# Kernel optimization log

Measured on AMD Instinct MI355X. Metric: run time of the kernel, lower is better.

The kernel has to match this reference:

```python
import jax, jax.numpy as jnp
import numpy as np
from jax import lax

SEQ, BATCH, IN, HID = 2048, 256, 64, 128


def setup_inputs() -> dict:
    key = jax.random.key(0)
    ks = jax.random.split(key, 5)
    return {
        "x": jax.random.normal(ks[0], (SEQ, BATCH, IN), dtype=jnp.float32),
        "Wx": jax.random.normal(ks[1], (HID, IN), dtype=jnp.float32) * 0.1,
        "bx": jax.random.normal(ks[2], (HID,), dtype=jnp.float32) * 0.1,
        "Wh": jax.random.normal(ks[3], (HID, HID), dtype=jnp.float32) * 0.1,
        "bh": jax.random.normal(ks[4], (HID,), dtype=jnp.float32) * 0.1,
    }


def reference(x, Wx, bx, Wh, bh):
    # Precompute the input projection for all timesteps in one GEMM:
    # fc_x(x[t]) + bh folded in. Shape (S, B, H).
    xp = jnp.einsum("sbi,hi->sbh", x, Wx) + bx + bh

    def step(h, xt):
        # h: (B, H); fc_h(h) = h @ Wh^T (bias folded into xp)
        h_new = jnp.tanh(h @ Wh.T + xt)
        return h_new, h_new

    h0 = jnp.zeros((x.shape[1], Wh.shape[0]), dtype=x.dtype)
    _, h_seq = lax.scan(step, h0, xp)  # (S, B, H)
    return h_seq, h_seq[-1][None]  # ((S,B,H), (1,B,H))
```

## Files before the change

### kernel.cpp

```cpp
#include <hip/hip_runtime.h>

#define SEQ   2048
#define BATCH 256
#define INDIM 64
#define HID   128

struct F2 { float x, y; };

template <int CTRL>
__device__ __forceinline__ float dpp_get(float v) {
    int t = __builtin_amdgcn_update_dpp(0, __builtin_bit_cast(int, v),
                                        CTRL, 0xF, 0xF, true);
    return __builtin_bit_cast(float, t);
}

#define PK_MUL(d, a, b) asm("v_pk_mul_f32 %0, %1, %2"     : "=v"(d) : "v"(a), "v"(b))
#define PK_FMA(d, a, b) asm("v_pk_fma_f32 %0, %1, %2, %0" : "+v"(d) : "v"(a), "v"(b))

#define TANH_K (-2.885390081777927f)
__device__ __forceinline__ float tanh_pre(float d, float bias_k) {
    float m = __builtin_fmaf(d, TANH_K, bias_k);
    float e = __builtin_amdgcn_exp2f(m);
    return (1.0f - e) * __builtin_amdgcn_rcpf(1.0f + e);
}

__global__ __launch_bounds__(512)
__attribute__((amdgpu_waves_per_eu(2, 2)))
void rnn_fused(
    const float* __restrict__ x,
    const float* __restrict__ Wx,
    const float* __restrict__ bx,
    const float* __restrict__ Wh,
    const float* __restrict__ bh,
    float* __restrict__ out)
{
    const int b   = blockIdx.x;
    const int tid = threadIdx.x;
    const int l   = tid & 63;
    const int w   = tid >> 6;
    const int s   = l & 15;
    const int j0  = w * 16 + (l >> 4) * 4;

    __shared__ __align__(16) float hbuf[2][HID];

    const double* WhD = (const double*)Wh;
    const double* WxD = (const double*)Wx;
    double wA[4], wB[4], wC[4], wD[4], wX[4], wY[4];
#pragma unroll
    for (int o = 0; o < 4; ++o) {
        const int row = j0 + (o ^ (l & 3));
        const int r   = row * 64 + 2 * s;
        wA[o] = WhD[r];      wB[o] = WhD[r + 1];
        wC[o] = WhD[r + 32]; wD[o] = WhD[r + 33];
        const int rx  = row * 32 + 2 * s;
        wX[o] = WxD[rx];     wY[o] = WxD[rx + 1];
    }
    const int jj = j0 + (l & 3);
    float bias_k = (bx[jj] + bh[jj]) * TANH_K;

    if (tid < 256) hbuf[tid >> 7][tid & 127] = 0.0f;
    __syncthreads();

    const double2* xb2 = (const double2*)(x + (size_t)b * INDIM + 4 * s);
    const size_t   S2  = (size_t)BATCH * INDIM / 4;
    double2 xa[4], xn[4];
#pragma unroll
    for (int i = 0; i < 4; ++i) xa[i] = xb2[(size_t)i * S2];

    float* outp = out + (size_t)b * HID + jj;
    const bool wr = (s < 4);
    float hv = 0.0f;

    for (int tb = 0; tb < SEQ; tb += 4) {
        asm volatile("" : "+v"(wA[0]), "+v"(wA[1]), "+v"(wA[2]), "+v"(wA[3]));
        asm volatile("" : "+v"(wB[0]), "+v"(wB[1]), "+v"(wB[2]), "+v"(wB[3]));
        asm volatile("" : "+v"(wC[0]), "+v"(wC[1]), "+v"(wC[2]), "+v"(wC[3]));
        asm volatile("" : "+v"(wD[0]), "+v"(wD[1]), "+v"(wD[2]), "+v"(wD[3]));
        asm volatile("" : "+v"(wX[0]), "+v"(wX[1]), "+v"(wX[2]), "+v"(wX[3]));
        asm volatile("" : "+v"(wY[0]), "+v"(wY[1]), "+v"(wY[2]), "+v"(wY[3]));
        asm volatile("" : "+v"(bias_k));

#pragma unroll
        for (int i = 0; i < 4; ++i) {
            int tp = tb + 4 + i; if (tp > SEQ - 1) tp = SEQ - 1;
            xn[i] = xb2[(size_t)tp * S2];
        }

#pragma unroll
        for (int q = 0; q < 4; ++q) {
            const double2* hbd = (const double2*)&hbuf[q & 1][0];

            const double2 H0 = hbd[s];
            const double2 H1 = hbd[16 + s];
            const double2 X  = xa[q];

            double acc0, acc1, acc2, acc3;
            PK_MUL(acc0, X.x, wX[0]); PK_MUL(acc1, X.x, wX[1]);
            PK_MUL(acc2, X.x, wX[2]); PK_MUL(acc3, X.x, wX[3]);
            PK_FMA(acc0, X.y, wY[0]); PK_FMA(acc1, X.y, wY[1]);
            PK_FMA(acc2, X.y, wY[2]); PK_FMA(acc3, X.y, wY[3]);
            PK_FMA(acc0, H0.x, wA[0]); PK_FMA(acc1, H0.x, wA[1]);
            PK_FMA(acc2, H0.x, wA[2]); PK_FMA(acc3, H0.x, wA[3]);
            PK_FMA(acc0, H0.y, wB[0]); PK_FMA(acc1, H0.y, wB[1]);
            PK_FMA(acc2, H0.y, wB[2]); PK_FMA(acc3, H0.y, wB[3]);
            PK_FMA(acc0, H1.x, wC[0]); PK_FMA(acc1, H1.x, wC[1]);
            PK_FMA(acc2, H1.x, wC[2]); PK_FMA(acc3, H1.x, wC[3]);
            PK_FMA(acc0, H1.y, wD[0]); PK_FMA(acc1, H1.y, wD[1]);
            PK_FMA(acc2, H1.y, wD[2]); PK_FMA(acc3, H1.y, wD[3]);

            float a0, a1, a2, a3;
            { F2 u = __builtin_bit_cast(F2, acc0); a0 = u.x + u.y; }
            { F2 u = __builtin_bit_cast(F2, acc1); a1 = u.x + u.y; }
            { F2 u = __builtin_bit_cast(F2, acc2); a2 = u.x + u.y; }
            { F2 u = __builtin_bit_cast(F2, acc3); a3 = u.x + u.y; }

            float c0 = a0 + dpp_get<0xB1>(a1);
            float c1 = a2 + dpp_get<0xB1>(a3);
            float d  = c0 + dpp_get<0x4E>(c1);
            d += dpp_get<0x124>(d);
            d += dpp_get<0x128>(d);

            hv = tanh_pre(d, bias_k);

            if (wr) {
                hbuf[(q + 1) & 1][jj] = hv;
                *outp = hv;
            }
            outp += BATCH * HID;

            asm volatile("s_waitcnt lgkmcnt(0)" ::: "memory");
            asm volatile("s_barrier" ::: "memory");
        }

#pragma unroll
        for (int i = 0; i < 4; ++i) xa[i] = xn[i];
    }

    if (wr)
        out[(size_t)SEQ * BATCH * HID + (size_t)b * HID + jj] = hv;
}

extern "C" void kernel_launch(void* const* d_in, const int* in_sizes, int n_in,
                              void* d_out, int out_size, void* d_ws, size_t ws_size,
                              hipStream_t stream) {
    const float* x  = (const float*)d_in[0];
    const float* Wx = (const float*)d_in[1];
    const float* bx = (const float*)d_in[2];
    const float* Wh = (const float*)d_in[3];
    const float* bh = (const float*)d_in[4];
    float* out = (float*)d_out;
    (void)in_sizes; (void)n_in; (void)d_ws; (void)ws_size; (void)out_size;
    rnn_fused<<<dim3(BATCH), dim3(512), 0, stream>>>(x, Wx, bx, Wh, bh, out);
}
```

Baseline: 607.8 us.

## Process two batch rows per block to share register-resident weights

Each block now handles two batch elements, interleaving their independent FMA chains, reductions and tanh so the same register-held Wh/Wx weights serve both rows, and launches half as many blocks. This aims to raise instruction-level parallelism inside the latency-bound serial recurrence and to cut the per-step barrier cost per batch row. The trade-off is twice the per-step arithmetic per block and higher register pressure, with only 128 blocks on a device that has 256 CUs, so part of the GPU sits idle.

```diff
diff --git a/kernel.cpp b/kernel.cpp
--- a/kernel.cpp
+++ b/kernel.cpp
@@ -34,14 +34,14 @@
     const float* __restrict__ bh,
     float* __restrict__ out)
 {
-    const int b   = blockIdx.x;
+    const int b0  = blockIdx.x * 2;
     const int tid = threadIdx.x;
     const int l   = tid & 63;
     const int w   = tid >> 6;
     const int s   = l & 15;
     const int j0  = w * 16 + (l >> 4) * 4;
 
-    __shared__ __align__(16) float hbuf[2][HID];
+    __shared__ __align__(16) float hbuf[2][2][HID];
 
     const double* WhD = (const double*)Wh;
     const double* WxD = (const double*)Wx;
@@ -58,18 +58,22 @@
     const int jj = j0 + (l & 3);
     float bias_k = (bx[jj] + bh[jj]) * TANH_K;
 
-    if (tid < 256) hbuf[tid >> 7][tid & 127] = 0.0f;
+    ((float*)hbuf)[tid] = 0.0f;
     __syncthreads();
 
-    const double2* xb2 = (const double2*)(x + (size_t)b * INDIM + 4 * s);
-    const size_t   S2  = (size_t)BATCH * INDIM / 4;
-    double2 xa[4], xn[4];
+    const double2* xb2a = (const double2*)(x + (size_t)b0 * INDIM + 4 * s);
+    const double2* xb2b = (const double2*)(x + (size_t)(b0 + 1) * INDIM + 4 * s);
+    const size_t   S2   = (size_t)BATCH * INDIM / 4;
+    double2 xaA[4], xnA[4], xaB[4], xnB[4];
 #pragma unroll
-    for (int i = 0; i < 4; ++i) xa[i] = xb2[(size_t)i * S2];
+    for (int i = 0; i < 4; ++i) {
+        xaA[i] = xb2a[(size_t)i * S2];
+        xaB[i] = xb2b[(size_t)i * S2];
+    }
 
-    float* outp = out + (size_t)b * HID + jj;
+    float* outp = out + (size_t)b0 * HID + jj;
     const bool wr = (s < 4);
-    float hv = 0.0f;
+    float hvA = 0.0f, hvB = 0.0f;
 
     for (int tb = 0; tb < SEQ; tb += 4) {
         asm volatile("" : "+v"(wA[0]), "+v"(wA[1]), "+v"(wA[2]), "+v"(wA[3]));
@@ -83,48 +87,78 @@
 #pragma unroll
         for (int i = 0; i < 4; ++i) {
             int tp = tb + 4 + i; if (tp > SEQ - 1) tp = SEQ - 1;
-            xn[i] = xb2[(size_t)tp * S2];
+            xnA[i] = xb2a[(size_t)tp * S2];
+            xnB[i] = xb2b[(size_t)tp * S2];
         }
 
 #pragma unroll
         for (int q = 0; q < 4; ++q) {
-            const double2* hbd = (const double2*)&hbuf[q & 1][0];
+            const double2* hbdA = (const double2*)&hbuf[0][q & 1][0];
+            const double2* hbdB = (const double2*)&hbuf[1][q & 1][0];
 
-            const double2 H0 = hbd[s];
-            const double2 H1 = hbd[16 + s];
-            const double2 X  = xa[q];
+            const double2 H0A = hbdA[s];
+            const double2 H1A = hbdA[16 + s];
+            const double2 H0B = hbdB[s];
+            const double2 H1B = hbdB[16 + s];
+            const double2 XA  = xaA[q];
+            const double2 XB  = xaB[q];
 
-            double acc0, acc1, acc2, acc3;
-            PK_MUL(acc0, X.x, wX[0]); PK_MUL(acc1, X.x, wX[1]);
-            PK_MUL(acc2, X.x, wX[2]); PK_MUL(acc3, X.x, wX[3]);
-            PK_FMA(acc0, X.y, wY[0]); PK_FMA(acc1, X.y, wY[1]);
-            PK_FMA(acc2, X.y, wY[2]); PK_FMA(acc3, X.y, wY[3]);
-            PK_FMA(acc0, H0.x, wA[0]); PK_FMA(acc1, H0.x, wA[1]);
-            PK_FMA(acc2, H0.x, wA[2]); PK_FMA(acc3, H0.x, wA[3]);
-            PK_FMA(acc0, H0.y, wB[0]); PK_FMA(acc1, H0.y, wB[1]);
-            PK_FMA(acc2, H0.y, wB[2]); PK_FMA(acc3, H0.y, wB[3]);
-            PK_FMA(acc0, H1.x, wC[0]); PK_FMA(acc1, H1.x, wC[1]);
-            PK_FMA(acc2, H1.x, wC[2]); PK_FMA(acc3, H1.x, wC[3]);
-            PK_FMA(acc0, H1.y, wD[0]); PK_FMA(acc1, H1.y, wD[1]);
-            PK_FMA(acc2, H1.y, wD[2]); PK_FMA(acc3, H1.y, wD[3]);
+            double pa0, pa1, pa2, pa3;
+            double pb0, pb1, pb2, pb3;
+            PK_MUL(pa0, XA.x, wX[0]); PK_MUL(pb0, XB.x, wX[0]);
+            PK_MUL(pa1, XA.x, wX[1]); PK_MUL(pb1, XB.x, wX[1]);
+            PK_MUL(pa2, XA.x, wX[2]); PK_MUL(pb2, XB.x, wX[2]);
+            PK_MUL(pa3, XA.x, wX[3]); PK_MUL(pb3, XB.x, wX[3]);
+            PK_FMA(pa0, XA.y, wY[0]); PK_FMA(pb0, XB.y, wY[0]);
+            PK_FMA(pa1, XA.y, wY[1]); PK_FMA(pb1, XB.y, wY[1]);
+            PK_FMA(pa2, XA.y, wY[2]); PK_FMA(pb2, XB.y, wY[2]);
+            PK_FMA(pa3, XA.y, wY[3]); PK_FMA(pb3, XB.y, wY[3]);
+            PK_FMA(pa0, H0A.x, wA[0]); PK_FMA(pb0, H0B.x, wA[0]);
+            PK_FMA(pa1, H0A.x, wA[1]); PK_FMA(pb1, H0B.x, wA[1]);
+            PK_FMA(pa2, H0A.x, wA[2]); PK_FMA(pb2, H0B.x, wA[2]);
+            PK_FMA(pa3, H0A.x, wA[3]); PK_FMA(pb3, H0B.x, wA[3]);
+            PK_FMA(pa0, H0A.y, wB[0]); PK_FMA(pb0, H0B.y, wB[0]);
+            PK_FMA(pa1, H0A.y, wB[1]); PK_FMA(pb1, H0B.y, wB[1]);
+            PK_FMA(pa2, H0A.y, wB[2]); PK_FMA(pb2, H0B.y, wB[2]);
+            PK_FMA(pa3, H0A.y, wB[3]); PK_FMA(pb3, H0B.y, wB[3]);
+            PK_FMA(pa0, H1A.x, wC[0]); PK_FMA(pb0, H1B.x, wC[0]);
+            PK_FMA(pa1, H1A.x, wC[1]); PK_FMA(pb1, H1B.x, wC[1]);
+            PK_FMA(pa2, H1A.x, wC[2]); PK_FMA(pb2, H1B.x, wC[2]);
+            PK_FMA(pa3, H1A.x, wC[3]); PK_FMA(pb3, H1B.x, wC[3]);
+            PK_FMA(pa0, H1A.y, wD[0]); PK_FMA(pb0, H1B.y, wD[0]);
+            PK_FMA(pa1, H1A.y, wD[1]); PK_FMA(pb1, H1B.y, wD[1]);
+            PK_FMA(pa2, H1A.y, wD[2]); PK_FMA(pb2, H1B.y, wD[2]);
+            PK_FMA(pa3, H1A.y, wD[3]); PK_FMA(pb3, H1B.y, wD[3]);
 
-            float a0, a1, a2, a3;
-            { F2 u = __builtin_bit_cast(F2, acc0); a0 = u.x + u.y; }
-            { F2 u = __builtin_bit_cast(F2, acc1); a1 = u.x + u.y; }
-            { F2 u = __builtin_bit_cast(F2, acc2); a2 = u.x + u.y; }
-            { F2 u = __builtin_bit_cast(F2, acc3); a3 = u.x + u.y; }
+            float aA0, aA1, aA2, aA3, aB0, aB1, aB2, aB3;
+            { F2 u = __builtin_bit_cast(F2, pa0); aA0 = u.x + u.y; }
+            { F2 u = __builtin_bit_cast(F2, pa1); aA1 = u.x + u.y; }
+            { F2 u = __builtin_bit_cast(F2, pa2); aA2 = u.x + u.y; }
+            { F2 u = __builtin_bit_cast(F2, pa3); aA3 = u.x + u.y; }
+            { F2 u = __builtin_bit_cast(F2, pb0); aB0 = u.x + u.y; }
+            { F2 u = __builtin_bit_cast(F2, pb1); aB1 = u.x + u.y; }
+            { F2 u = __builtin_bit_cast(F2, pb2); aB2 = u.x + u.y; }
+            { F2 u = __builtin_bit_cast(F2, pb3); aB3 = u.x + u.y; }
 
-            float c0 = a0 + dpp_get<0xB1>(a1);
-            float c1 = a2 + dpp_get<0xB1>(a3);
-            float d  = c0 + dpp_get<0x4E>(c1);
-            d += dpp_get<0x124>(d);
-            d += dpp_get<0x128>(d);
+            float cA0 = aA0 + dpp_get<0xB1>(aA1);
+            float cB0 = aB0 + dpp_get<0xB1>(aB1);
+            float cA1 = aA2 + dpp_get<0xB1>(aA3);
+            float cB1 = aB2 + dpp_get<0xB1>(aB3);
+            float dA  = cA0 + dpp_get<0x4E>(cA1);
+            float dB  = cB0 + dpp_get<0x4E>(cB1);
+            dA += dpp_get<0x124>(dA);
+            dB += dpp_get<0x124>(dB);
+            dA += dpp_get<0x128>(dA);
+            dB += dpp_get<0x128>(dB);
 
-            hv = tanh_pre(d, bias_k);
+            hvA = tanh_pre(dA, bias_k);
+            hvB = tanh_pre(dB, bias_k);
 
             if (wr) {
-                hbuf[(q + 1) & 1][jj] = hv;
-                *outp = hv;
+                hbuf[0][(q + 1) & 1][jj] = hvA;
+                hbuf[1][(q + 1) & 1][jj] = hvB;
+                *outp        = hvA;
+                *(outp + HID) = hvB;
             }
             outp += BATCH * HID;
 
@@ -133,11 +167,13 @@
         }
 
 #pragma unroll
-        for (int i = 0; i < 4; ++i) xa[i] = xn[i];
+        for (int i = 0; i < 4; ++i) { xaA[i] = xnA[i]; xaB[i] = xnB[i]; }
     }
 
-    if (wr)
-        out[(size_t)SEQ * BATCH * HID + (size_t)b * HID + jj] = hv;
+    if (wr) {
+        out[(size_t)SEQ * BATCH * HID + (size_t)b0 * HID + jj]       = hvA;
+        out[(size_t)SEQ * BATCH * HID + (size_t)(b0 + 1) * HID + jj] = hvB;
+    }
 }
 
 extern "C" void kernel_launch(void* const* d_in, const int* in_sizes, int n_in,
@@ -150,5 +186,5 @@
     const float* bh = (const float*)d_in[4];
     float* out = (float*)d_out;
     (void)in_sizes; (void)n_in; (void)d_ws; (void)ws_size; (void)out_size;
-    rnn_fused<<<dim3(BATCH), dim3(512), 0, stream>>>(x, Wx, bx, Wh, bh, out);
+    rnn_fused<<<dim3(BATCH / 2), dim3(512), 0, stream>>>(x, Wx, bx, Wh, bh, out);
 }
```

New measurement: 1.095 ms. 80.2% more time.

## Halve block size so each thread computes two hidden outputs per step

Applied to the files above, without the earlier changes.

The work split changes from 512 threads with 4 output rows per 16-lane group to 256 threads with 8 rows, so each lane computes two hidden units per timestep. With 4 waves per block instead of 8, the per-step s_barrier has fewer waves to synchronize. The cost is double the register footprint for weights (96 VGPR doubles) and twice the serial FMA work per lane on the latency-critical recurrent path. Occupancy is now pinned at 1 wave per EU.

```diff
diff --git a/kernel.cpp b/kernel.cpp
--- a/kernel.cpp
+++ b/kernel.cpp
@@ -24,8 +24,8 @@
     return (1.0f - e) * __builtin_amdgcn_rcpf(1.0f + e);
 }
 
-__global__ __launch_bounds__(512)
-__attribute__((amdgpu_waves_per_eu(2, 2)))
+__global__ __launch_bounds__(256)
+__attribute__((amdgpu_waves_per_eu(1, 1)))
 void rnn_fused(
     const float* __restrict__ x,
     const float* __restrict__ Wx,
@@ -39,26 +39,27 @@
     const int l   = tid & 63;
     const int w   = tid >> 6;
     const int s   = l & 15;
-    const int j0  = w * 16 + (l >> 4) * 4;
+    const int j0  = w * 32 + (l >> 4) * 8;
 
     __shared__ __align__(16) float hbuf[2][HID];
 
     const double* WhD = (const double*)Wh;
     const double* WxD = (const double*)Wx;
-    double wA[4], wB[4], wC[4], wD[4], wX[4], wY[4];
+    double wA[8], wB[8], wC[8], wD[8], wX[8], wY[8];
 #pragma unroll
-    for (int o = 0; o < 4; ++o) {
-        const int row = j0 + (o ^ (l & 3));
+    for (int o = 0; o < 8; ++o) {
+        const int row = j0 + (o & 4) + ((o & 3) ^ (l & 3));
         const int r   = row * 64 + 2 * s;
         wA[o] = WhD[r];      wB[o] = WhD[r + 1];
         wC[o] = WhD[r + 32]; wD[o] = WhD[r + 33];
         const int rx  = row * 32 + 2 * s;
         wX[o] = WxD[rx];     wY[o] = WxD[rx + 1];
     }
-    const int jj = j0 + (l & 3);
-    float bias_k = (bx[jj] + bh[jj]) * TANH_K;
+    const int jj  = j0 + (l & 3);
+    float bias_k  = (bx[jj]     + bh[jj])     * TANH_K;
+    float bias_k2 = (bx[jj + 4] + bh[jj + 4]) * TANH_K;
 
-    if (tid < 256) hbuf[tid >> 7][tid & 127] = 0.0f;
+    ((float*)hbuf)[tid] = 0.0f;
     __syncthreads();
 
     const double2* xb2 = (const double2*)(x + (size_t)b * INDIM + 4 * s);
@@ -69,16 +70,22 @@
 
     float* outp = out + (size_t)b * HID + jj;
     const bool wr = (s < 4);
-    float hv = 0.0f;
+    float hv1 = 0.0f, hv2 = 0.0f;
 
     for (int tb = 0; tb < SEQ; tb += 4) {
-        asm volatile("" : "+v"(wA[0]), "+v"(wA[1]), "+v"(wA[2]), "+v"(wA[3]));
-        asm volatile("" : "+v"(wB[0]), "+v"(wB[1]), "+v"(wB[2]), "+v"(wB[3]));
-        asm volatile("" : "+v"(wC[0]), "+v"(wC[1]), "+v"(wC[2]), "+v"(wC[3]));
-        asm volatile("" : "+v"(wD[0]), "+v"(wD[1]), "+v"(wD[2]), "+v"(wD[3]));
-        asm volatile("" : "+v"(wX[0]), "+v"(wX[1]), "+v"(wX[2]), "+v"(wX[3]));
-        asm volatile("" : "+v"(wY[0]), "+v"(wY[1]), "+v"(wY[2]), "+v"(wY[3]));
-        asm volatile("" : "+v"(bias_k));
+        asm volatile("" : "+v"(wA[0]), "+v"(wA[1]), "+v"(wA[2]), "+v"(wA[3]),
+                          "+v"(wA[4]), "+v"(wA[5]), "+v"(wA[6]), "+v"(wA[7]));
+        asm volatile("" : "+v"(wB[0]), "+v"(wB[1]), "+v"(wB[2]), "+v"(wB[3]),
+                          "+v"(wB[4]), "+v"(wB[5]), "+v"(wB[6]), "+v"(wB[7]));
+        asm volatile("" : "+v"(wC[0]), "+v"(wC[1]), "+v"(wC[2]), "+v"(wC[3]),
+                          "+v"(wC[4]), "+v"(wC[5]), "+v"(wC[6]), "+v"(wC[7]));
+        asm volatile("" : "+v"(wD[0]), "+v"(wD[1]), "+v"(wD[2]), "+v"(wD[3]),
+                          "+v"(wD[4]), "+v"(wD[5]), "+v"(wD[6]), "+v"(wD[7]));
+        asm volatile("" : "+v"(wX[0]), "+v"(wX[1]), "+v"(wX[2]), "+v"(wX[3]),
+                          "+v"(wX[4]), "+v"(wX[5]), "+v"(wX[6]), "+v"(wX[7]));
+        asm volatile("" : "+v"(wY[0]), "+v"(wY[1]), "+v"(wY[2]), "+v"(wY[3]),
+                          "+v"(wY[4]), "+v"(wY[5]), "+v"(wY[6]), "+v"(wY[7]));
+        asm volatile("" : "+v"(bias_k), "+v"(bias_k2));
 
 #pragma unroll
         for (int i = 0; i < 4; ++i) {
@@ -94,37 +101,49 @@
             const double2 H1 = hbd[16 + s];
             const double2 X  = xa[q];
 
-            double acc0, acc1, acc2, acc3;
-            PK_MUL(acc0, X.x, wX[0]); PK_MUL(acc1, X.x, wX[1]);
-            PK_MUL(acc2, X.x, wX[2]); PK_MUL(acc3, X.x, wX[3]);
-            PK_FMA(acc0, X.y, wY[0]); PK_FMA(acc1, X.y, wY[1]);
-            PK_FMA(acc2, X.y, wY[2]); PK_FMA(acc3, X.y, wY[3]);
-            PK_FMA(acc0, H0.x, wA[0]); PK_FMA(acc1, H0.x, wA[1]);
-            PK_FMA(acc2, H0.x, wA[2]); PK_FMA(acc3, H0.x, wA[3]);
-            PK_FMA(acc0, H0.y, wB[0]); PK_FMA(acc1, H0.y, wB[1]);
-            PK_FMA(acc2, H0.y, wB[2]); PK_FMA(acc3, H0.y, wB[3]);
-            PK_FMA(acc0, H1.x, wC[0]); PK_FMA(acc1, H1.x, wC[1]);
-            PK_FMA(acc2, H1.x, wC[2]); PK_FMA(acc3, H1.x, wC[3]);
-            PK_FMA(acc0, H1.y, wD[0]); PK_FMA(acc1, H1.y, wD[1]);
-            PK_FMA(acc2, H1.y, wD[2]); PK_FMA(acc3, H1.y, wD[3]);
+            double acc[8];
+#pragma unroll
+            for (int o = 0; o < 8; ++o) PK_MUL(acc[o], X.x, wX[o]);
+#pragma unroll
+            for (int o = 0; o < 8; ++o) PK_FMA(acc[o], X.y, wY[o]);
+#pragma unroll
+            for (int o = 0; o < 8; ++o) PK_FMA(acc[o], H0.x, wA[o]);
+#pragma unroll
+            for (int o = 0; o < 8; ++o) PK_FMA(acc[o], H0.y, wB[o]);
+#pragma unroll
+            for (int o = 0; o < 8; ++o) PK_FMA(acc[o], H1.x, wC[o]);
+#pragma unroll
+            for (int o = 0; o < 8; ++o) PK_FMA(acc[o], H1.y, wD[o]);
 
-            float a0, a1, a2, a3;
-            { F2 u = __builtin_bit_cast(F2, acc0); a0 = u.x + u.y; }
-            { F2 u = __builtin_bit_cast(F2, acc1); a1 = u.x + u.y; }
-            { F2 u = __builtin_bit_cast(F2, acc2); a2 = u.x + u.y; }
-            { F2 u = __builtin_bit_cast(F2, acc3); a3 = u.x + u.y; }
+            float a0, a1, a2, a3, a4, a5, a6, a7;
+            { F2 u = __builtin_bit_cast(F2, acc[0]); a0 = u.x + u.y; }
+            { F2 u = __builtin_bit_cast(F2, acc[1]); a1 = u.x + u.y; }
+            { F2 u = __builtin_bit_cast(F2, acc[2]); a2 = u.x + u.y; }
+            { F2 u = __builtin_bit_cast(F2, acc[3]); a3 = u.x + u.y; }
+            { F2 u = __builtin_bit_cast(F2, acc[4]); a4 = u.x + u.y; }
+            { F2 u = __builtin_bit_cast(F2, acc[5]); a5 = u.x + u.y; }
+            { F2 u = __builtin_bit_cast(F2, acc[6]); a6 = u.x + u.y; }
+            { F2 u = __builtin_bit_cast(F2, acc[7]); a7 = u.x + u.y; }
 
             float c0 = a0 + dpp_get<0xB1>(a1);
+            float c2 = a4 + dpp_get<0xB1>(a5);
             float c1 = a2 + dpp_get<0xB1>(a3);
-            float d  = c0 + dpp_get<0x4E>(c1);
-            d += dpp_get<0x124>(d);
-            d += dpp_get<0x128>(d);
+            float c3 = a6 + dpp_get<0xB1>(a7);
+            float d1 = c0 + dpp_get<0x4E>(c1);
+            float d2 = c2 + dpp_get<0x4E>(c3);
+            d1 += dpp_get<0x124>(d1);
+            d2 += dpp_get<0x124>(d2);
+            d1 += dpp_get<0x128>(d1);
+            d2 += dpp_get<0x128>(d2);
 
-            hv = tanh_pre(d, bias_k);
+            hv1 = tanh_pre(d1, bias_k);
+            hv2 = tanh_pre(d2, bias_k2);
 
             if (wr) {
-                hbuf[(q + 1) & 1][jj] = hv;
-                *outp = hv;
+                hbuf[(q + 1) & 1][jj]     = hv1;
+                hbuf[(q + 1) & 1][jj + 4] = hv2;
+                outp[0] = hv1;
+                outp[4] = hv2;
             }
             outp += BATCH * HID;
 
@@ -136,8 +155,10 @@
         for (int i = 0; i < 4; ++i) xa[i] = xn[i];
     }
 
-    if (wr)
-        out[(size_t)SEQ * BATCH * HID + (size_t)b * HID + jj] = hv;
+    if (wr) {
+        out[(size_t)SEQ * BATCH * HID + (size_t)b * HID + jj]     = hv1;
+        out[(size_t)SEQ * BATCH * HID + (size_t)b * HID + jj + 4] = hv2;
+    }
 }
 
 extern "C" void kernel_launch(void* const* d_in, const int* in_sizes, int n_in,
@@ -150,5 +171,5 @@
     const float* bh = (const float*)d_in[4];
     float* out = (float*)d_out;
     (void)in_sizes; (void)n_in; (void)d_ws; (void)ws_size; (void)out_size;
-    rnn_fused<<<dim3(BATCH), dim3(512), 0, stream>>>(x, Wx, bx, Wh, bh, out);
+    rnn_fused<<<dim3(BATCH), dim3(256), 0, stream>>>(x, Wx, bx, Wh, bh, out);
 }
```

Result: slower. 633.1 us (+4.2%).
